# Optimization experiments

Hardware: AMD Instinct MI355X
Metric: run time of the kernel (lower is better)

Reference implementation:

```python
import jax, jax.numpy as jnp
import numpy as np

B = 8192      # batch
T = 8         # obs_len
E = 256       # feature_dim
M = 20        # num_modes
NH = 4        # attention heads
HD = E // NH  # head dim
FS = 12       # future_steps
LN_EPS = 1e-5


def setup_inputs() -> dict:
    key = jax.random.key(0)
    ks = jax.random.split(key, 32)
    s = 0.05
    def n(i, shape):
        return jax.random.normal(ks[i], shape, jnp.float32) * s
    return {
        "observed_trajectory": jax.random.normal(ks[0], (B, T, 2), jnp.float32),
        # 2-layer LSTM (torch gate order i,f,g,o)
        "w_ih0": n(1, (4 * E, 2)), "w_hh0": n(2, (4 * E, E)),
        "b_ih0": n(3, (4 * E,)), "b_hh0": n(4, (4 * E,)),
        "w_ih1": n(5, (4 * E, E)), "w_hh1": n(6, (4 * E, E)),
        "b_ih1": n(7, (4 * E,)), "b_hh1": n(8, (4 * E,)),
        # 20 MHA modules, weights stacked over mode axis
        "in_proj_w": n(9, (M, 3 * E, E)), "in_proj_b": n(10, (M, 3 * E)),
        "out_w": n(11, (M, E, E)), "out_b": n(12, (M, E)),
        # FFN: LN -> Linear(256,1024) -> ReLU -> Linear(1024,256) -> LN
        "ln1_g": jnp.ones((E,)), "ln1_b": jnp.zeros((E,)),
        "ffn_w1": n(13, (1024, E)), "ffn_b1": n(14, (1024,)),
        "ffn_w2": n(15, (E, 1024)), "ffn_b2": n(16, (E,)),
        "ln2_g": jnp.ones((E,)), "ln2_b": jnp.zeros((E,)),
        # decoder MLP
        "dec_w1": n(17, (512, E)), "dec_b1": n(18, (512,)),
        "dec_w2": n(19, (FS * 2, 512)), "dec_b2": n(20, (FS * 2,)),
        # scorer MLP
        "sc_w1": n(21, (128, E)), "sc_b1": n(22, (128,)),
        "sc_w2": n(23, (1, 128)), "sc_b2": n(24, (1,)),
    }


def _lstm_layer(xs, w_ih, w_hh, b_ih, b_hh):
    # xs: (T, B, in_dim) -> (ys (T,B,E), h_T (B,E))
    bb = xs.shape[1]
    h0 = jnp.zeros((bb, E), xs.dtype)
    c0 = jnp.zeros((bb, E), xs.dtype)
    def step(carry, x):
        h, c = carry
        g = x @ w_ih.T + h @ w_hh.T + b_ih + b_hh
        i, f, gg, o = jnp.split(g, 4, axis=-1)
        c = jax.nn.sigmoid(f) * c + jax.nn.sigmoid(i) * jnp.tanh(gg)
        h = jax.nn.sigmoid(o) * jnp.tanh(c)
        return (h, c), h
    (h_t, _), ys = jax.lax.scan(step, (h0, c0), xs)
    return ys, h_t


def _ln(x, g, b):
    m = jnp.mean(x, -1, keepdims=True)
    v = jnp.mean((x - m) ** 2, -1, keepdims=True)
    return (x - m) * jax.lax.rsqrt(v + LN_EPS) * g + b


def _forward(observed_trajectory, w_ih0, w_hh0, b_ih0, b_hh0,
             w_ih1, w_hh1, b_ih1, b_hh1,
             in_proj_w, in_proj_b, out_w, out_b,
             ln1_g, ln1_b, ffn_w1, ffn_b1, ffn_w2, ffn_b2, ln2_g, ln2_b,
             dec_w1, dec_b1, dec_w2, dec_b2,
             sc_w1, sc_b1, sc_w2, sc_b2):
    bsz = observed_trajectory.shape[0]
    # --- TrajectoryEncoder: 2-layer LSTM, take last-step output of layer 2 ---
    xs = jnp.transpose(observed_trajectory, (1, 0, 2))  # (T, B, 2)
    ys0, _ = _lstm_layer(xs, w_ih0, w_hh0, b_ih0, b_hh0)
    _, emb = _lstm_layer(ys0, w_ih1, w_hh1, b_ih1, b_hh1)  # (B, E)

    # --- MultiModalTransformer: 20 MHA modules on seq_len=1 (fused over modes) ---
    # query == key == value == emb. Dropout is eval-mode identity.
    qkv = jnp.einsum('be,mfe->bmf', emb, in_proj_w) + in_proj_b  # (B, M, 3E)
    q, k, v = jnp.split(qkv, 3, axis=-1)
    q = q.reshape(bsz, M, NH, HD)
    k = k.reshape(bsz, M, NH, HD)
    v = v.reshape(bsz, M, NH, HD)
    # kv length is 1 -> softmax over a single score is identically 1
    scores = jnp.sum(q * k, -1, keepdims=True) / jnp.sqrt(jnp.float32(HD))  # (B,M,NH,1)
    attn = jax.nn.softmax(scores, axis=-1)
    ctx = (attn * v).reshape(bsz, M, E)
    attn_out = jnp.einsum('bmf,mof->bmo', ctx, out_w) + out_b  # (B, M, E)
    # FFN (no residual in original module)
    h = _ln(attn_out, ln1_g, ln1_b)
    h = jax.nn.relu(h @ ffn_w1.T + ffn_b1)
    h = h @ ffn_w2.T + ffn_b2
    mm_emb = _ln(h, ln2_g, ln2_b)  # (B, M, E)

    # --- TrajectoryDecoder ---
    last_pos = observed_trajectory[:, -1, :]  # (B, 2)
    d = jax.nn.elu(mm_emb @ dec_w1.T + dec_b1)
    deltas = (d @ dec_w2.T + dec_b2).reshape(bsz, M, FS, 2)
    predictions = deltas + last_pos[:, None, None, :]

    # --- ModeScorer ---
    s = jax.nn.elu(mm_emb @ sc_w1.T + sc_b1)
    scores_out = (s @ sc_w2.T + sc_b2)[..., 0]  # (B, M)
    return predictions, scores_out


def reference(observed_trajectory, w_ih0, w_hh0, b_ih0, b_hh0,
              w_ih1, w_hh1, b_ih1, b_hh1,
              in_proj_w, in_proj_b, out_w, out_b,
              ln1_g, ln1_b, ffn_w1, ffn_b1, ffn_w2, ffn_b2, ln2_g, ln2_b,
              dec_w1, dec_b1, dec_w2, dec_b2,
              sc_w1, sc_b1, sc_w2, sc_b2):
    return _forward(observed_trajectory, w_ih0, w_hh0, b_ih0, b_hh0,
                    w_ih1, w_hh1, b_ih1, b_hh1,
                    in_proj_w, in_proj_b, out_w, out_b,
                    ln1_g, ln1_b, ffn_w1, ffn_b1, ffn_w2, ffn_b2, ln2_g, ln2_b,
                    dec_w1, dec_b1, dec_w2, dec_b2,
                    sc_w1, sc_b1, sc_w2, sc_b2)
```

## Files before the change

### kernel.cpp

```cpp
#include <hip/hip_runtime.h>
#include <math.h>


typedef float4 f4;
typedef unsigned int u32;
typedef unsigned short u16;
typedef __attribute__((ext_vector_type(16))) float f32x16;
typedef __attribute__((ext_vector_type(8)))  short s16x8;

__device__ __forceinline__ float sigm(float x){ return 1.0f/(1.0f + __expf(-x)); }
__device__ __forceinline__ float tanhfast(float x){ return 2.0f*sigm(2.0f*x) - 1.0f; }
__device__ __forceinline__ float eluf(float x){ return x > 0.f ? x : expm1f(x); }
__device__ __forceinline__ u16 f2bf(float x){
  u32 u = __float_as_uint(x);
  return (u16)((u + 0x7FFFu + ((u>>16)&1u)) >> 16);
}
__device__ __forceinline__ float bf2f(u16 h){ return __uint_as_float(((u32)h)<<16); }


#define LSTR 264

__global__ __launch_bounds__(256, 4)
void w2c_kernel(const float* __restrict__ out_w, const float* __restrict__ ipw,
                float* __restrict__ W2c)
{
  __shared__ float As[16][68];
  __shared__ float Bs2[16][68];
  const int tid = threadIdx.x;
  const int m = blockIdx.y;
  const int o0 = (blockIdx.x >> 2) * 64, e0 = (blockIdx.x & 3) * 64;
  const int trow = tid >> 4, tcol = tid & 15;
  const float* Ap = out_w + (size_t)m * 65536;
  const float* Bp = ipw + ((size_t)m * 768 + 512) * 256;
  float acc[16];
#pragma unroll
  for (int z = 0; z < 16; ++z) acc[z] = 0.f;
  for (int kb = 0; kb < 256; kb += 16) {
    { int row = tid >> 2, ko = (tid & 3) * 4;
      f4 v = *(const f4*)(Ap + (size_t)(o0+row)*256 + kb + ko);
      As[ko+0][row]=v.x; As[ko+1][row]=v.y; As[ko+2][row]=v.z; As[ko+3][row]=v.w; }
    { int k = tid >> 4, eo = (tid & 15) * 4;
      *(f4*)&Bs2[k][eo] = *(const f4*)(Bp + (size_t)(kb+k)*256 + e0 + eo); }
    __syncthreads();
#pragma unroll
    for (int k = 0; k < 16; ++k) {
      f4 a4 = *(const f4*)&As[k][trow*4];
      f4 b4 = *(const f4*)&Bs2[k][tcol*4];
      acc[0]+=a4.x*b4.x; acc[1]+=a4.x*b4.y; acc[2]+=a4.x*b4.z; acc[3]+=a4.x*b4.w;
      acc[4]+=a4.y*b4.x; acc[5]+=a4.y*b4.y; acc[6]+=a4.y*b4.z; acc[7]+=a4.y*b4.w;
      acc[8]+=a4.z*b4.x; acc[9]+=a4.z*b4.y; acc[10]+=a4.z*b4.z; acc[11]+=a4.z*b4.w;
      acc[12]+=a4.w*b4.x; acc[13]+=a4.w*b4.y; acc[14]+=a4.w*b4.z; acc[15]+=a4.w*b4.w;
    }
    __syncthreads();
  }
#pragma unroll
  for (int i = 0; i < 4; ++i)
    *(f4*)&W2c[((size_t)m*256 + o0 + trow*4 + i)*256 + e0 + tcol*4] =
        make_float4(acc[i*4+0], acc[i*4+1], acc[i*4+2], acc[i*4+3]);
}

__global__ void b2c_kernel(const float* __restrict__ out_w, const float* __restrict__ out_b,
                           const float* __restrict__ ipb, float* __restrict__ b2c)
{
  __shared__ float pb[256];
  const int m = blockIdx.x, o = threadIdx.x;
  pb[o] = ipb[(size_t)m*768 + 512 + o];
  __syncthreads();
  const float* wr = out_w + ((size_t)m*256 + o)*256;
  float acc = out_b[(size_t)m*256 + o];
  for (int f = 0; f < 256; f += 4) {
    f4 w = *(const f4*)&wr[f];
    acc += w.x*pb[f] + w.y*pb[f+1] + w.z*pb[f+2] + w.w*pb[f+3];
  }
  b2c[(size_t)m*256 + o] = acc;
}

__device__ __forceinline__ void cvt_seg(const float* __restrict__ src, u16* __restrict__ dst,
                                        int Creal, int lognks, int g)
{
  const int l = g & 63;
  const int cks = g >> 6;
  const int ks = cks & ((1 << lognks) - 1);
  const int ct = cks >> lognks;
  const int c = ct*32 + (l & 31);
  const int K = 16 << lognks;
  const int k = ks*16 + ((l >> 5) * 8);
  s16x8 r;
  if (c < Creal) {
    const float* s = src + (size_t)c * K + k;
    f4 v0 = *(const f4*)s;
    f4 v1 = *(const f4*)(s + 4);
    r[0]=(short)f2bf(v0.x); r[1]=(short)f2bf(v0.y); r[2]=(short)f2bf(v0.z); r[3]=(short)f2bf(v0.w);
    r[4]=(short)f2bf(v1.x); r[5]=(short)f2bf(v1.y); r[6]=(short)f2bf(v1.z); r[7]=(short)f2bf(v1.w);
  } else {
#pragma unroll
    for (int j = 0; j < 8; ++j) r[j] = 0;
  }
  *(s16x8*)(dst + (size_t)g * 8) = r;
}

__global__ __launch_bounds__(256)
void wcvt_all(const float* __restrict__ whh0, const float* __restrict__ wih1,
              const float* __restrict__ whh1, const float* __restrict__ W2c,
              const float* __restrict__ ffn1, const float* __restrict__ ffn2,
              const float* __restrict__ dec1, const float* __restrict__ dec2,
              const float* __restrict__ sc1,  u16* __restrict__ dst)
{
  int g = blockIdx.x * 256 + threadIdx.x;
  if      (g <  32768) cvt_seg(whh0, dst + 0,       1024, 4, g);
  else if (g <  65536) cvt_seg(wih1, dst + 262144,  1024, 4, g - 32768);
  else if (g <  98304) cvt_seg(whh1, dst + 524288,  1024, 4, g - 65536);
  else if (g < 262144) cvt_seg(W2c,  dst + 786432,  5120, 4, g - 98304);
  else if (g < 294912) cvt_seg(ffn1, dst + 2097152, 1024, 4, g - 262144);
  else if (g < 327680) cvt_seg(ffn2, dst + 2359296,  256, 6, g - 294912);
  else if (g < 344064) cvt_seg(dec1, dst + 2621440,  512, 4, g - 327680);
  else if (g < 346112) cvt_seg(dec2, dst + 2752512,   24, 5, g - 344064);
  else if (g < 350208) cvt_seg(sc1,  dst + 2768896,  128, 4, g - 346112);
}

__global__ __launch_bounds__(512, 2)
void lstm_fused(const u16* __restrict__ whh0f, const u16* __restrict__ wih1f,
                const u16* __restrict__ whh1f, const float* __restrict__ w_ih0,
                const float* __restrict__ b_ih0, const float* __restrict__ b_hh0,
                const float* __restrict__ b_ih1, const float* __restrict__ b_hh1,
                const float* __restrict__ obs, u16* __restrict__ emb)
{
  __shared__ u16 h0s[32 * LSTR];
  __shared__ u16 h1s[32 * LSTR];
  __shared__ float obs_s[512];
  const int tid = threadIdx.x;
  const int lane = tid & 63, w = tid >> 6;
  const int col = lane & 31, hi = lane >> 5;
  const int r0 = blockIdx.x * 32;
  if (tid < 512) obs_s[tid] = obs[(size_t)r0 * 16 + tid];

  float bs0[4], bs1[4], xw0[4], xw1[4];
#pragma unroll
  for (int g = 0; g < 4; ++g) {
    const int cg = g*256 + w*32 + col;
    bs0[g] = b_ih0[cg] + b_hh0[cg];
    bs1[g] = b_ih1[cg] + b_hh1[cg];
    xw0[g] = w_ih0[2*cg];
    xw1[g] = w_ih0[2*cg + 1];
  }
  float c0v[16], c1v[16];
#pragma unroll
  for (int r = 0; r < 16; ++r) { c0v[r] = 0.f; c1v[r] = 0.f; }

  f32x16 za;
#pragma unroll
  for (int i = 0; i < 16; ++i) za[i] = 0.f;

  __syncthreads();

  for (int t = 0; t < 8; ++t) {
    f32x16 accA[4], accB[4];
#pragma unroll
    for (int g = 0; g < 4; ++g) { accA[g] = za; accB[g] = za; }
    if (t > 0) {
#pragma unroll 2
      for (int ks = 0; ks < 16; ++ks) {
        s16x8 a0 = *(const s16x8*)(h0s + col*LSTR + ks*16 + hi*8);
        s16x8 a1 = *(const s16x8*)(h1s + col*LSTR + ks*16 + hi*8);
#pragma unroll
        for (int g = 0; g < 4; ++g) {
          const size_t fo = ((size_t)((g*8 + w)*16 + ks)*64 + lane)*8;
          s16x8 bA = *(const s16x8*)(whh0f + fo);
          accA[g] = __builtin_amdgcn_mfma_f32_32x32x16_bf16(a0, bA, accA[g], 0, 0, 0);
          s16x8 bB = *(const s16x8*)(whh1f + fo);
          accB[g] = __builtin_amdgcn_mfma_f32_32x32x16_bf16(a1, bB, accB[g], 0, 0, 0);
        }
      }
    }
    __syncthreads();
#pragma unroll
    for (int r = 0; r < 16; ++r) {
      const int row = (r&3) + 8*(r>>2) + 4*hi;
      const float x0 = obs_s[row*16 + 2*t], x1 = obs_s[row*16 + 2*t + 1];
      const float gi = accA[0][r] + bs0[0] + x0*xw0[0] + x1*xw1[0];
      const float gf = accA[1][r] + bs0[1] + x0*xw0[1] + x1*xw1[1];
      const float gg = accA[2][r] + bs0[2] + x0*xw0[2] + x1*xw1[2];
      const float go = accA[3][r] + bs0[3] + x0*xw0[3] + x1*xw1[3];
      const float cn = sigm(gf)*c0v[r] + sigm(gi)*tanhfast(gg);
      c0v[r] = cn;
      h0s[row*LSTR + w*32 + col] = f2bf(sigm(go)*tanhfast(cn));
    }
    __syncthreads();
#pragma unroll 4
    for (int ks = 0; ks < 16; ++ks) {
      s16x8 a = *(const s16x8*)(h0s + col*LSTR + ks*16 + hi*8);
#pragma unroll
      for (int g = 0; g < 4; ++g) {
        s16x8 b = *(const s16x8*)(wih1f + ((size_t)((g*8 + w)*16 + ks)*64 + lane)*8);
        accB[g] = __builtin_amdgcn_mfma_f32_32x32x16_bf16(a, b, accB[g], 0, 0, 0);
      }
    }
#pragma unroll
    for (int r = 0; r < 16; ++r) {
      const int row = (r&3) + 8*(r>>2) + 4*hi;
      const float gi = accB[0][r] + bs1[0];
      const float gf = accB[1][r] + bs1[1];
      const float gg = accB[2][r] + bs1[2];
      const float go = accB[3][r] + bs1[3];
      const float cn = sigm(gf)*c1v[r] + sigm(gi)*tanhfast(gg);
      c1v[r] = cn;
      h1s[row*LSTR + w*32 + col] = f2bf(sigm(go)*tanhfast(cn));
    }
    __syncthreads();
  }
#pragma unroll
  for (int kk = 0; kk < 2; ++kk) {
    const int gi2 = tid + kk*512;
    const int row = gi2 >> 5, grp = gi2 & 31;
    *(s16x8*)(emb + (size_t)(r0 + row)*256 + grp*8) = *(const s16x8*)(h1s + row*LSTR + grp*8);
  }
}

__device__ __forceinline__ void gemm128(const u16* As, const u16* __restrict__ Bf,
                                        f32x16 acc[2], int ct, int rh, int lane)
{
  const int col = lane & 31, hi = lane >> 5;
#pragma unroll 4
  for (int ks = 0; ks < 16; ++ks) {
    s16x8 b = *(const s16x8*)(Bf + ((size_t)(ct*16 + ks)*64 + lane)*8);
#pragma unroll
    for (int i = 0; i < 2; ++i) {
      s16x8 a = *(const s16x8*)(As + ((rh*2 + i)*32 + col)*LSTR + ks*16 + hi*8);
      acc[i] = __builtin_amdgcn_mfma_f32_32x32x16_bf16(a, b, acc[i], 0, 0, 0);
    }
  }
}

__device__ __forceinline__ void gemm_ffn2_128(const u16* As, const u16* __restrict__ Bf,
                                              f32x16 acc[2], int c4, int ct, int rh, int lane)
{
  const int col = lane & 31, hi = lane >> 5;
#pragma unroll 4
  for (int ks = 0; ks < 16; ++ks) {
    s16x8 b = *(const s16x8*)(Bf + ((size_t)(ct*64 + c4*16 + ks)*64 + lane)*8);
#pragma unroll
    for (int i = 0; i < 2; ++i) {
      s16x8 a = *(const s16x8*)(As + ((rh*2 + i)*32 + col)*LSTR + ks*16 + hi*8);
      acc[i] = __builtin_amdgcn_mfma_f32_32x32x16_bf16(a, b, acc[i], 0, 0, 0);
    }
  }
}

template<int ACT>
__device__ __forceinline__ void epi_store128(f32x16 acc[2], const float* __restrict__ bias,
                                             u16* Ys, int ct, int rh, int lane)
{
  const int col = lane & 31, hi = lane >> 5, cg = ct*32 + col;
  const float bv = bias[cg];
#pragma unroll
  for (int i = 0; i < 2; ++i)
#pragma unroll
    for (int r = 0; r < 16; ++r) {
      float v = acc[i][r] + bv;
      if (ACT == 1) v = fmaxf(v, 0.f);
      else if (ACT == 2) v = eluf(v);
      const int row = (rh*2 + i)*32 + (r&3) + 8*(r>>2) + 4*hi;
      Ys[row*LSTR + cg] = f2bf(v);
    }
}

__device__ __forceinline__ void lnpass128(const u16* In, u16* Out,
    const float* __restrict__ g, const float* __restrict__ b, int tid)
{
  const int lane = tid & 63, w = tid >> 6;
  f4 gv = *(const f4*)&g[lane*4];
  f4 bv = *(const f4*)&b[lane*4];
#pragma unroll
  for (int i = 0; i < 8; ++i) {
    const int row = w*8 + i;
    ushort4 uv = *(const ushort4*)(In + row*LSTR + lane*4);
    float v0 = bf2f(uv.x), v1 = bf2f(uv.y), v2 = bf2f(uv.z), v3 = bf2f(uv.w);
    float s  = v0 + v1 + v2 + v3;
    float ss = v0*v0 + v1*v1 + v2*v2 + v3*v3;
#pragma unroll
    for (int d = 1; d < 64; d <<= 1) { s += __shfl_xor(s, d); ss += __shfl_xor(ss, d); }
    const float mean = s * (1.f/256.f);
    const float rs = rsqrtf(ss * (1.f/256.f) - mean*mean + 1e-5f);
    ushort4 o;
    o.x = f2bf((v0 - mean)*rs*gv.x + bv.x);
    o.y = f2bf((v1 - mean)*rs*gv.y + bv.y);
    o.z = f2bf((v2 - mean)*rs*gv.z + bv.z);
    o.w = f2bf((v3 - mean)*rs*gv.w + bv.w);
    *(ushort4*)(Out + row*LSTR + lane*4) = o;
  }
}

__global__ __launch_bounds__(1024, 4)
void mode_stack(const u16* __restrict__ emb, const u16* __restrict__ W2cf,
  const float* __restrict__ b2c,
  const float* __restrict__ ln1_g, const float* __restrict__ ln1_b,
  const u16* __restrict__ ffn1f, const float* __restrict__ ffn_b1,
  const u16* __restrict__ ffn2f, const float* __restrict__ ffn_b2,
  const float* __restrict__ ln2_g, const float* __restrict__ ln2_b,
  const u16* __restrict__ dec1f, const float* __restrict__ dec_b1,
  const u16* __restrict__ dec2f, const float* __restrict__ dec_b2,
  const u16* __restrict__ sc1f,  const float* __restrict__ sc_b1,
  const float* __restrict__ sc_w2, const float* __restrict__ sc_b2,
  const float* __restrict__ obs, float* __restrict__ pred, float* __restrict__ score)
{
  __shared__ u16 Xs[128 * LSTR];
  __shared__ u16 Ys[128 * LSTR];
  __shared__ float obs_ls[256];
  const int tid = threadIdx.x;
  const int lane = tid & 63, w = tid >> 6;
  const int ct = w & 7, rh = w >> 3;
  const int col = lane & 31, hi = lane >> 5;
  const int r0 = blockIdx.x * 128;
  const int m  = blockIdx.y;

  f32x16 za;
#pragma unroll
  for (int i = 0; i < 16; ++i) za[i] = 0.f;

#pragma unroll
  for (int kk = 0; kk < 4; ++kk) {
    const int gi2 = tid + kk*1024;
    const int row = gi2 >> 5, grp = gi2 & 31;
    *(s16x8*)(Xs + row*LSTR + grp*8) = *(const s16x8*)(emb + (size_t)(r0 + row)*256 + grp*8);
  }
  if (tid < 256) obs_ls[tid] = obs[(size_t)(r0 + (tid >> 1))*16 + 14 + (tid & 1)];
  __syncthreads();

  {
    f32x16 acc[2]; acc[0] = za; acc[1] = za;
    gemm128(Xs, W2cf + (size_t)m*65536, acc, ct, rh, lane);
    epi_store128<0>(acc, b2c + m*256, Ys, ct, rh, lane);
  }
  __syncthreads();
  lnpass128(Ys, Xs, ln1_g, ln1_b, tid);
  __syncthreads();

  f32x16 h2[2]; h2[0] = za; h2[1] = za;
  for (int c4 = 0; c4 < 4; ++c4) {
    f32x16 tacc[2]; tacc[0] = za; tacc[1] = za;
    gemm128(Xs, ffn1f + (size_t)c4*65536, tacc, ct, rh, lane);
    epi_store128<1>(tacc, ffn_b1 + c4*256, Ys, ct, rh, lane);
    __syncthreads();
    gemm_ffn2_128(Ys, ffn2f, h2, c4, ct, rh, lane);
    __syncthreads();
  }
  epi_store128<0>(h2, ffn_b2, Ys, ct, rh, lane);
  __syncthreads();
  lnpass128(Ys, Xs, ln2_g, ln2_b, tid);
  __syncthreads();

  f32x16 dv[2]; dv[0] = za; dv[1] = za;
  for (int c2 = 0; c2 < 2; ++c2) {
    f32x16 tacc[2]; tacc[0] = za; tacc[1] = za;
    gemm128(Xs, dec1f + (size_t)c2*65536, tacc, ct, rh, lane);
    epi_store128<2>(tacc, dec_b1 + c2*256, Ys, ct, rh, lane);
    __syncthreads();
    if (ct == 0) {
#pragma unroll 4
      for (int ks = 0; ks < 16; ++ks) {
        s16x8 b = *(const s16x8*)(dec2f + ((size_t)(c2*16 + ks)*64 + lane)*8);
#pragma unroll
        for (int i = 0; i < 2; ++i) {
          s16x8 a = *(const s16x8*)(Ys + ((rh*2 + i)*32 + col)*LSTR + ks*16 + hi*8);
          dv[i] = __builtin_amdgcn_mfma_f32_32x32x16_bf16(a, b, dv[i], 0, 0, 0);
        }
      }
    }
    __syncthreads();
  }
  if (ct == 0 && col < 24) {
    const float db = dec_b2[col];
#pragma unroll
    for (int i = 0; i < 2; ++i)
#pragma unroll
      for (int r = 0; r < 16; ++r) {
        const int row = (rh*2 + i)*32 + (r&3) + 8*(r>>2) + 4*hi;
        const float lp = obs_ls[row*2 + (col & 1)];
        pred[((size_t)(r0 + row)*20 + m)*24 + col] = dv[i][r] + db + lp;
      }
  }

  if (ct < 4) {
    f32x16 sacc[2]; sacc[0] = za; sacc[1] = za;
    gemm128(Xs, sc1f, sacc, ct, rh, lane);
    epi_store128<2>(sacc, sc_b1, Ys, ct, rh, lane);
  }
  __syncthreads();
  {
    const float scb2 = sc_b2[0];
    const float2 w2v = *(const float2*)&sc_w2[lane*2];
#pragma unroll
    for (int i = 0; i < 8; ++i) {
      const int row = w*8 + i;
      u32 pv = *(const u32*)(Ys + row*LSTR + lane*2);
      float part = bf2f((u16)(pv & 0xFFFF))*w2v.x + bf2f((u16)(pv >> 16))*w2v.y;
#pragma unroll
      for (int d = 1; d < 64; d <<= 1) part += __shfl_xor(part, d);
      if (lane == 0) score[(size_t)(r0 + row)*20 + m] = part + scb2;
    }
  }
}

extern "C" void kernel_launch(void* const* d_in, const int* in_sizes, int n_in,
                              void* d_out, int out_size, void* d_ws, size_t ws_size,
                              hipStream_t stream)
{
  (void)in_sizes; (void)n_in; (void)out_size; (void)ws_size;
  const float* obs    = (const float*)d_in[0];
  const float* w_ih0  = (const float*)d_in[1];
  const float* w_hh0  = (const float*)d_in[2];
  const float* b_ih0  = (const float*)d_in[3];
  const float* b_hh0  = (const float*)d_in[4];
  const float* w_ih1  = (const float*)d_in[5];
  const float* w_hh1  = (const float*)d_in[6];
  const float* b_ih1  = (const float*)d_in[7];
  const float* b_hh1  = (const float*)d_in[8];
  const float* ipw    = (const float*)d_in[9];
  const float* ipb    = (const float*)d_in[10];
  const float* out_w  = (const float*)d_in[11];
  const float* out_b  = (const float*)d_in[12];
  const float* ln1_g  = (const float*)d_in[13];
  const float* ln1_b  = (const float*)d_in[14];
  const float* ffn_w1 = (const float*)d_in[15];
  const float* ffn_b1 = (const float*)d_in[16];
  const float* ffn_w2 = (const float*)d_in[17];
  const float* ffn_b2 = (const float*)d_in[18];
  const float* ln2_g  = (const float*)d_in[19];
  const float* ln2_b  = (const float*)d_in[20];
  const float* dec_w1 = (const float*)d_in[21];
  const float* dec_b1 = (const float*)d_in[22];
  const float* dec_w2 = (const float*)d_in[23];
  const float* dec_b2 = (const float*)d_in[24];
  const float* sc_w1  = (const float*)d_in[25];
  const float* sc_b1  = (const float*)d_in[26];
  const float* sc_w2  = (const float*)d_in[27];
  const float* sc_b2  = (const float*)d_in[28];

  float* outp   = (float*)d_out;
  float* pred   = outp;
  float* scoreo = outp + (size_t)8192*20*24;

  float* wsf   = (float*)d_ws;
  float* W2c   = wsf;
  float* b2cp  = wsf + 1310720;
  u16*   wsh   = (u16*)(wsf + 1315840);
  u16* whh0f = wsh + 0;
  u16* wih1f = wsh + 262144;
  u16* whh1f = wsh + 524288;
  u16* W2cf  = wsh + 786432;
  u16* ffn1f = wsh + 2097152;
  u16* ffn2f = wsh + 2359296;
  u16* dec1f = wsh + 2621440;
  u16* dec2f = wsh + 2752512;
  u16* sc1f  = wsh + 2768896;
  u16* emb   = wsh + 2801664;

  w2c_kernel<<<dim3(16, 20), 256, 0, stream>>>(out_w, ipw, W2c);
  b2c_kernel<<<20, 256, 0, stream>>>(out_w, out_b, ipb, b2cp);
  wcvt_all<<<1368, 256, 0, stream>>>(w_hh0, w_ih1, w_hh1, W2c, ffn_w1, ffn_w2,
                                     dec_w1, dec_w2, sc_w1, wsh);
  lstm_fused<<<256, 512, 0, stream>>>(whh0f, wih1f, whh1f, w_ih0, b_ih0, b_hh0,
                                      b_ih1, b_hh1, obs, emb);
  mode_stack<<<dim3(64, 20), 1024, 0, stream>>>(emb, W2cf, b2cp,
      ln1_g, ln1_b, ffn1f, ffn_b1, ffn2f, ffn_b2, ln2_g, ln2_b,
      dec1f, dec_b1, dec2f, dec_b2, sc1f, sc_b1, sc_w2, sc_b2,
      obs, pred, scoreo);
}
```

Baseline: 811.3 us.

## Halve mode_stack row tile, restructure LSTM schedule to cut register pressure

The mode_stack kernel now processes 64 rows per block instead of 128, with one accumulator per wave and twice as many blocks, and raises launch bounds so more blocks fit per CU. The LSTM kernel is reordered so layer 0 completes before layer 1. Layer 1 accumulates its input and recurrent products into a single accumulator set, and its cell state is kept in shared memory instead of registers, which lets the launch bound rise to 4. ELU switches from expm1f to __expf-1. The costs are more weight reloads per row, a larger LDS footprint in the LSTM kernel, extra barriers, and slightly less accurate ELU near zero.

```diff
diff --git a/kernel.cpp b/kernel.cpp
--- a/kernel.cpp
+++ b/kernel.cpp
@@ -10,7 +10,7 @@
 
 __device__ __forceinline__ float sigm(float x){ return 1.0f/(1.0f + __expf(-x)); }
 __device__ __forceinline__ float tanhfast(float x){ return 2.0f*sigm(2.0f*x) - 1.0f; }
-__device__ __forceinline__ float eluf(float x){ return x > 0.f ? x : expm1f(x); }
+__device__ __forceinline__ float eluf(float x){ return x > 0.f ? x : __expf(x) - 1.0f; }
 __device__ __forceinline__ u16 f2bf(float x){
   u32 u = __float_as_uint(x);
   return (u16)((u + 0x7FFFu + ((u>>16)&1u)) >> 16);
@@ -118,7 +118,7 @@
   else if (g < 350208) cvt_seg(sc1,  dst + 2768896,  128, 4, g - 346112);
 }
 
-__global__ __launch_bounds__(512, 2)
+__global__ __launch_bounds__(512, 4)
 void lstm_fused(const u16* __restrict__ whh0f, const u16* __restrict__ wih1f,
                 const u16* __restrict__ whh1f, const float* __restrict__ w_ih0,
                 const float* __restrict__ b_ih0, const float* __restrict__ b_hh0,
@@ -127,12 +127,13 @@
 {
   __shared__ u16 h0s[32 * LSTR];
   __shared__ u16 h1s[32 * LSTR];
+  __shared__ float c1ls[32 * 256];
   __shared__ float obs_s[512];
   const int tid = threadIdx.x;
   const int lane = tid & 63, w = tid >> 6;
   const int col = lane & 31, hi = lane >> 5;
   const int r0 = blockIdx.x * 32;
-  if (tid < 512) obs_s[tid] = obs[(size_t)r0 * 16 + tid];
+  obs_s[tid] = obs[(size_t)r0 * 16 + tid];
 
   float bs0[4], bs1[4], xw0[4], xw1[4];
 #pragma unroll
@@ -143,9 +144,9 @@
     xw0[g] = w_ih0[2*cg];
     xw1[g] = w_ih0[2*cg + 1];
   }
-  float c0v[16], c1v[16];
-#pragma unroll
-  for (int r = 0; r < 16; ++r) { c0v[r] = 0.f; c1v[r] = 0.f; }
+  float c0v[16];
+#pragma unroll
+  for (int r = 0; r < 16; ++r) c0v[r] = 0.f;
 
   f32x16 za;
 #pragma unroll
@@ -154,9 +155,36 @@
   __syncthreads();
 
   for (int t = 0; t < 8; ++t) {
-    f32x16 accA[4], accB[4];
-#pragma unroll
-    for (int g = 0; g < 4; ++g) { accA[g] = za; accB[g] = za; }
+    f32x16 acc[4];
+#pragma unroll
+    for (int g = 0; g < 4; ++g) acc[g] = za;
+    if (t > 0) {
+#pragma unroll 4
+      for (int ks = 0; ks < 16; ++ks) {
+        s16x8 a = *(const s16x8*)(h0s + col*LSTR + ks*16 + hi*8);
+#pragma unroll
+        for (int g = 0; g < 4; ++g) {
+          s16x8 b = *(const s16x8*)(whh0f + ((size_t)((g*8 + w)*16 + ks)*64 + lane)*8);
+          acc[g] = __builtin_amdgcn_mfma_f32_32x32x16_bf16(a, b, acc[g], 0, 0, 0);
+        }
+      }
+    }
+    __syncthreads();
+#pragma unroll
+    for (int r = 0; r < 16; ++r) {
+      const int row = (r&3) + 8*(r>>2) + 4*hi;
+      const float x0 = obs_s[row*16 + 2*t], x1 = obs_s[row*16 + 2*t + 1];
+      const float gi = acc[0][r] + bs0[0] + x0*xw0[0] + x1*xw1[0];
+      const float gf = acc[1][r] + bs0[1] + x0*xw0[1] + x1*xw1[1];
+      const float gg = acc[2][r] + bs0[2] + x0*xw0[2] + x1*xw1[2];
+      const float go = acc[3][r] + bs0[3] + x0*xw0[3] + x1*xw1[3];
+      const float cn = sigm(gf)*c0v[r] + sigm(gi)*tanhfast(gg);
+      c0v[r] = cn;
+      h0s[row*LSTR + w*32 + col] = f2bf(sigm(go)*tanhfast(cn));
+    }
+    __syncthreads();
+#pragma unroll
+    for (int g = 0; g < 4; ++g) acc[g] = za;
     if (t > 0) {
 #pragma unroll 2
       for (int ks = 0; ks < 16; ++ks) {
@@ -165,46 +193,36 @@
 #pragma unroll
         for (int g = 0; g < 4; ++g) {
           const size_t fo = ((size_t)((g*8 + w)*16 + ks)*64 + lane)*8;
-          s16x8 bA = *(const s16x8*)(whh0f + fo);
-          accA[g] = __builtin_amdgcn_mfma_f32_32x32x16_bf16(a0, bA, accA[g], 0, 0, 0);
-          s16x8 bB = *(const s16x8*)(whh1f + fo);
-          accB[g] = __builtin_amdgcn_mfma_f32_32x32x16_bf16(a1, bB, accB[g], 0, 0, 0);
+          s16x8 b0 = *(const s16x8*)(wih1f + fo);
+          acc[g] = __builtin_amdgcn_mfma_f32_32x32x16_bf16(a0, b0, acc[g], 0, 0, 0);
+          s16x8 b1 = *(const s16x8*)(whh1f + fo);
+          acc[g] = __builtin_amdgcn_mfma_f32_32x32x16_bf16(a1, b1, acc[g], 0, 0, 0);
         }
       }
+    } else {
+#pragma unroll 4
+      for (int ks = 0; ks < 16; ++ks) {
+        s16x8 a0 = *(const s16x8*)(h0s + col*LSTR + ks*16 + hi*8);
+#pragma unroll
+        for (int g = 0; g < 4; ++g) {
+          s16x8 b0 = *(const s16x8*)(wih1f + ((size_t)((g*8 + w)*16 + ks)*64 + lane)*8);
+          acc[g] = __builtin_amdgcn_mfma_f32_32x32x16_bf16(a0, b0, acc[g], 0, 0, 0);
+        }
+      }
     }
     __syncthreads();
 #pragma unroll
     for (int r = 0; r < 16; ++r) {
       const int row = (r&3) + 8*(r>>2) + 4*hi;
-      const float x0 = obs_s[row*16 + 2*t], x1 = obs_s[row*16 + 2*t + 1];
-      const float gi = accA[0][r] + bs0[0] + x0*xw0[0] + x1*xw1[0];
-      const float gf = accA[1][r] + bs0[1] + x0*xw0[1] + x1*xw1[1];
-      const float gg = accA[2][r] + bs0[2] + x0*xw0[2] + x1*xw1[2];
-      const float go = accA[3][r] + bs0[3] + x0*xw0[3] + x1*xw1[3];
-      const float cn = sigm(gf)*c0v[r] + sigm(gi)*tanhfast(gg);
-      c0v[r] = cn;
-      h0s[row*LSTR + w*32 + col] = f2bf(sigm(go)*tanhfast(cn));
-    }
-    __syncthreads();
-#pragma unroll 4
-    for (int ks = 0; ks < 16; ++ks) {
-      s16x8 a = *(const s16x8*)(h0s + col*LSTR + ks*16 + hi*8);
-#pragma unroll
-      for (int g = 0; g < 4; ++g) {
-        s16x8 b = *(const s16x8*)(wih1f + ((size_t)((g*8 + w)*16 + ks)*64 + lane)*8);
-        accB[g] = __builtin_amdgcn_mfma_f32_32x32x16_bf16(a, b, accB[g], 0, 0, 0);
-      }
-    }
-#pragma unroll
-    for (int r = 0; r < 16; ++r) {
-      const int row = (r&3) + 8*(r>>2) + 4*hi;
-      const float gi = accB[0][r] + bs1[0];
-      const float gf = accB[1][r] + bs1[1];
-      const float gg = accB[2][r] + bs1[2];
-      const float go = accB[3][r] + bs1[3];
-      const float cn = sigm(gf)*c1v[r] + sigm(gi)*tanhfast(gg);
-      c1v[r] = cn;
-      h1s[row*LSTR + w*32 + col] = f2bf(sigm(go)*tanhfast(cn));
+      const int e = w*32 + col;
+      const float gi = acc[0][r] + bs1[0];
+      const float gf = acc[1][r] + bs1[1];
+      const float gg = acc[2][r] + bs1[2];
+      const float go = acc[3][r] + bs1[3];
+      const float cold = (t > 0) ? c1ls[row*256 + e] : 0.f;
+      const float cn = sigm(gf)*cold + sigm(gi)*tanhfast(gg);
+      c1ls[row*256 + e] = cn;
+      h1s[row*LSTR + e] = f2bf(sigm(go)*tanhfast(cn));
     }
     __syncthreads();
   }
@@ -216,63 +234,55 @@
   }
 }
 
-__device__ __forceinline__ void gemm128(const u16* As, const u16* __restrict__ Bf,
-                                        f32x16 acc[2], int ct, int rh, int lane)
+__device__ __forceinline__ void gemm64(const u16* As, const u16* __restrict__ Bf,
+                                       f32x16& acc, int ct, int rh, int lane)
 {
   const int col = lane & 31, hi = lane >> 5;
-#pragma unroll 4
+#pragma unroll 8
   for (int ks = 0; ks < 16; ++ks) {
     s16x8 b = *(const s16x8*)(Bf + ((size_t)(ct*16 + ks)*64 + lane)*8);
-#pragma unroll
-    for (int i = 0; i < 2; ++i) {
-      s16x8 a = *(const s16x8*)(As + ((rh*2 + i)*32 + col)*LSTR + ks*16 + hi*8);
-      acc[i] = __builtin_amdgcn_mfma_f32_32x32x16_bf16(a, b, acc[i], 0, 0, 0);
-    }
-  }
-}
-
-__device__ __forceinline__ void gemm_ffn2_128(const u16* As, const u16* __restrict__ Bf,
-                                              f32x16 acc[2], int c4, int ct, int rh, int lane)
+    s16x8 a = *(const s16x8*)(As + (rh*32 + col)*LSTR + ks*16 + hi*8);
+    acc = __builtin_amdgcn_mfma_f32_32x32x16_bf16(a, b, acc, 0, 0, 0);
+  }
+}
+
+__device__ __forceinline__ void gemm_ffn2_64(const u16* As, const u16* __restrict__ Bf,
+                                             f32x16& acc, int c4, int ct, int rh, int lane)
 {
   const int col = lane & 31, hi = lane >> 5;
-#pragma unroll 4
+#pragma unroll 8
   for (int ks = 0; ks < 16; ++ks) {
     s16x8 b = *(const s16x8*)(Bf + ((size_t)(ct*64 + c4*16 + ks)*64 + lane)*8);
-#pragma unroll
-    for (int i = 0; i < 2; ++i) {
-      s16x8 a = *(const s16x8*)(As + ((rh*2 + i)*32 + col)*LSTR + ks*16 + hi*8);
-      acc[i] = __builtin_amdgcn_mfma_f32_32x32x16_bf16(a, b, acc[i], 0, 0, 0);
-    }
+    s16x8 a = *(const s16x8*)(As + (rh*32 + col)*LSTR + ks*16 + hi*8);
+    acc = __builtin_amdgcn_mfma_f32_32x32x16_bf16(a, b, acc, 0, 0, 0);
   }
 }
 
 template<int ACT>
-__device__ __forceinline__ void epi_store128(f32x16 acc[2], const float* __restrict__ bias,
-                                             u16* Ys, int ct, int rh, int lane)
+__device__ __forceinline__ void epi_store64(f32x16 acc, const float* __restrict__ bias,
+                                            u16* Ys, int ct, int rh, int lane)
 {
   const int col = lane & 31, hi = lane >> 5, cg = ct*32 + col;
   const float bv = bias[cg];
 #pragma unroll
-  for (int i = 0; i < 2; ++i)
-#pragma unroll
-    for (int r = 0; r < 16; ++r) {
-      float v = acc[i][r] + bv;
-      if (ACT == 1) v = fmaxf(v, 0.f);
-      else if (ACT == 2) v = eluf(v);
-      const int row = (rh*2 + i)*32 + (r&3) + 8*(r>>2) + 4*hi;
-      Ys[row*LSTR + cg] = f2bf(v);
-    }
-}
-
-__device__ __forceinline__ void lnpass128(const u16* In, u16* Out,
+  for (int r = 0; r < 16; ++r) {
+    float v = acc[r] + bv;
+    if (ACT == 1) v = fmaxf(v, 0.f);
+    else if (ACT == 2) v = eluf(v);
+    const int row = rh*32 + (r&3) + 8*(r>>2) + 4*hi;
+    Ys[row*LSTR + cg] = f2bf(v);
+  }
+}
+
+__device__ __forceinline__ void lnpass64(const u16* In, u16* Out,
     const float* __restrict__ g, const float* __restrict__ b, int tid)
 {
   const int lane = tid & 63, w = tid >> 6;
   f4 gv = *(const f4*)&g[lane*4];
   f4 bv = *(const f4*)&b[lane*4];
 #pragma unroll
-  for (int i = 0; i < 8; ++i) {
-    const int row = w*8 + i;
+  for (int i = 0; i < 4; ++i) {
+    const int row = w*4 + i;
     ushort4 uv = *(const ushort4*)(In + row*LSTR + lane*4);
     float v0 = bf2f(uv.x), v1 = bf2f(uv.y), v2 = bf2f(uv.z), v3 = bf2f(uv.w);
     float s  = v0 + v1 + v2 + v3;
@@ -290,7 +300,7 @@
   }
 }
 
-__global__ __launch_bounds__(1024, 4)
+__global__ __launch_bounds__(1024, 8)
 void mode_stack(const u16* __restrict__ emb, const u16* __restrict__ W2cf,
   const float* __restrict__ b2c,
   const float* __restrict__ ln1_g, const float* __restrict__ ln1_b,
@@ -303,14 +313,14 @@
   const float* __restrict__ sc_w2, const float* __restrict__ sc_b2,
   const float* __restrict__ obs, float* __restrict__ pred, float* __restrict__ score)
 {
-  __shared__ u16 Xs[128 * LSTR];
-  __shared__ u16 Ys[128 * LSTR];
-  __shared__ float obs_ls[256];
+  __shared__ u16 Xs[64 * LSTR];
+  __shared__ u16 Ys[64 * LSTR];
+  __shared__ float obs_ls[128];
   const int tid = threadIdx.x;
   const int lane = tid & 63, w = tid >> 6;
   const int ct = w & 7, rh = w >> 3;
   const int col = lane & 31, hi = lane >> 5;
-  const int r0 = blockIdx.x * 128;
+  const int r0 = blockIdx.x * 64;
   const int m  = blockIdx.y;
 
   f32x16 za;
@@ -318,52 +328,49 @@
   for (int i = 0; i < 16; ++i) za[i] = 0.f;
 
 #pragma unroll
-  for (int kk = 0; kk < 4; ++kk) {
+  for (int kk = 0; kk < 2; ++kk) {
     const int gi2 = tid + kk*1024;
     const int row = gi2 >> 5, grp = gi2 & 31;
     *(s16x8*)(Xs + row*LSTR + grp*8) = *(const s16x8*)(emb + (size_t)(r0 + row)*256 + grp*8);
   }
-  if (tid < 256) obs_ls[tid] = obs[(size_t)(r0 + (tid >> 1))*16 + 14 + (tid & 1)];
+  if (tid < 128) obs_ls[tid] = obs[(size_t)(r0 + (tid >> 1))*16 + 14 + (tid & 1)];
   __syncthreads();
 
   {
-    f32x16 acc[2]; acc[0] = za; acc[1] = za;
-    gemm128(Xs, W2cf + (size_t)m*65536, acc, ct, rh, lane);
-    epi_store128<0>(acc, b2c + m*256, Ys, ct, rh, lane);
-  }
-  __syncthreads();
-  lnpass128(Ys, Xs, ln1_g, ln1_b, tid);
-  __syncthreads();
-
-  f32x16 h2[2]; h2[0] = za; h2[1] = za;
+    f32x16 acc = za;
+    gemm64(Xs, W2cf + (size_t)m*65536, acc, ct, rh, lane);
+    epi_store64<0>(acc, b2c + m*256, Ys, ct, rh, lane);
+  }
+  __syncthreads();
+  lnpass64(Ys, Xs, ln1_g, ln1_b, tid);
+  __syncthreads();
+
+  f32x16 h2 = za;
   for (int c4 = 0; c4 < 4; ++c4) {
-    f32x16 tacc[2]; tacc[0] = za; tacc[1] = za;
-    gemm128(Xs, ffn1f + (size_t)c4*65536, tacc, ct, rh, lane);
-    epi_store128<1>(tacc, ffn_b1 + c4*256, Ys, ct, rh, lane);
-    __syncthreads();
-    gemm_ffn2_128(Ys, ffn2f, h2, c4, ct, rh, lane);
-    __syncthreads();
-  }
-  epi_store128<0>(h2, ffn_b2, Ys, ct, rh, lane);
-  __syncthreads();
-  lnpass128(Ys, Xs, ln2_g, ln2_b, tid);
-  __syncthreads();
-
-  f32x16 dv[2]; dv[0] = za; dv[1] = za;
+    f32x16 tacc = za;
+    gemm64(Xs, ffn1f + (size_t)c4*65536, tacc, ct, rh, lane);
+    epi_store64<1>(tacc, ffn_b1 + c4*256, Ys, ct, rh, lane);
+    __syncthreads();
+    gemm_ffn2_64(Ys, ffn2f, h2, c4, ct, rh, lane);
+    __syncthreads();
+  }
+  epi_store64<0>(h2, ffn_b2, Ys, ct, rh, lane);
+  __syncthreads();
+  lnpass64(Ys, Xs, ln2_g, ln2_b, tid);
+  __syncthreads();
+
+  f32x16 dv = za;
   for (int c2 = 0; c2 < 2; ++c2) {
-    f32x16 tacc[2]; tacc[0] = za; tacc[1] = za;
-    gemm128(Xs, dec1f + (size_t)c2*65536, tacc, ct, rh, lane);
-    epi_store128<2>(tacc, dec_b1 + c2*256, Ys, ct, rh, lane);
+    f32x16 tacc = za;
+    gemm64(Xs, dec1f + (size_t)c2*65536, tacc, ct, rh, lane);
+    epi_store64<2>(tacc, dec_b1 + c2*256, Ys, ct, rh, lane);
     __syncthreads();
     if (ct == 0) {
-#pragma unroll 4
+#pragma unroll 8
       for (int ks = 0; ks < 16; ++ks) {
         s16x8 b = *(const s16x8*)(dec2f + ((size_t)(c2*16 + ks)*64 + lane)*8);
-#pragma unroll
-        for (int i = 0; i < 2; ++i) {
-          s16x8 a = *(const s16x8*)(Ys + ((rh*2 + i)*32 + col)*LSTR + ks*16 + hi*8);
-          dv[i] = __builtin_amdgcn_mfma_f32_32x32x16_bf16(a, b, dv[i], 0, 0, 0);
-        }
+        s16x8 a = *(const s16x8*)(Ys + (rh*32 + col)*LSTR + ks*16 + hi*8);
+        dv = __builtin_amdgcn_mfma_f32_32x32x16_bf16(a, b, dv, 0, 0, 0);
       }
     }
     __syncthreads();
@@ -371,27 +378,25 @@
   if (ct == 0 && col < 24) {
     const float db = dec_b2[col];
 #pragma unroll
-    for (int i = 0; i < 2; ++i)
-#pragma unroll
-      for (int r = 0; r < 16; ++r) {
-        const int row = (rh*2 + i)*32 + (r&3) + 8*(r>>2) + 4*hi;
-        const float lp = obs_ls[row*2 + (col & 1)];
-        pred[((size_t)(r0 + row)*20 + m)*24 + col] = dv[i][r] + db + lp;
-      }
+    for (int r = 0; r < 16; ++r) {
+      const int row = rh*32 + (r&3) + 8*(r>>2) + 4*hi;
+      const float lp = obs_ls[row*2 + (col & 1)];
+      pred[((size_t)(r0 + row)*20 + m)*24 + col] = dv[r] + db + lp;
+    }
   }
 
   if (ct < 4) {
-    f32x16 sacc[2]; sacc[0] = za; sacc[1] = za;
-    gemm128(Xs, sc1f, sacc, ct, rh, lane);
-    epi_store128<2>(sacc, sc_b1, Ys, ct, rh, lane);
+    f32x16 sacc = za;
+    gemm64(Xs, sc1f, sacc, ct, rh, lane);
+    epi_store64<2>(sacc, sc_b1, Ys, ct, rh, lane);
   }
   __syncthreads();
   {
     const float scb2 = sc_b2[0];
     const float2 w2v = *(const float2*)&sc_w2[lane*2];
 #pragma unroll
-    for (int i = 0; i < 8; ++i) {
-      const int row = w*8 + i;
+    for (int i = 0; i < 4; ++i) {
+      const int row = w*4 + i;
       u32 pv = *(const u32*)(Ys + row*LSTR + lane*2);
       float part = bf2f((u16)(pv & 0xFFFF))*w2v.x + bf2f((u16)(pv >> 16))*w2v.y;
 #pragma unroll
@@ -461,7 +466,7 @@
                                      dec_w1, dec_w2, sc_w1, wsh);
   lstm_fused<<<256, 512, 0, stream>>>(whh0f, wih1f, whh1f, w_ih0, b_ih0, b_hh0,
                                       b_ih1, b_hh1, obs, emb);
-  mode_stack<<<dim3(64, 20), 1024, 0, stream>>>(emb, W2cf, b2cp,
+  mode_stack<<<dim3(128, 20), 1024, 0, stream>>>(emb, W2cf, b2cp,
       ln1_g, ln1_b, ffn1f, ffn_b1, ffn2f, ffn_b2, ln2_g, ln2_b,
       dec1f, dec_b1, dec2f, dec_b2, sc1f, sc_b1, sc_w2, sc_b2,
       obs, pred, scoreo);
```

Result: slower. 1.356 ms (+67.1%).
